# Kernel tuning notes

Measured on AMD Instinct MI355X. Metric: run time of the kernel, lower is better.

## Reference

```python
import jax, jax.numpy as jnp
import numpy as np

NUM_CHARTS = 64
LATENT_DIM = 128
CURVATURE = 1.0
MAX_NORM = 0.99
EPS = 1e-15


def _project_to_ball(z):
    # clamp norm to MAX_NORM (project to interior of Poincare ball)
    norm = jnp.linalg.norm(z, axis=-1, keepdims=True)
    return jnp.where(norm > MAX_NORM, z * (MAX_NORM / norm), z)


def _mobius_add(x, y, c):
    x2 = jnp.sum(x * x, axis=-1, keepdims=True)
    y2 = jnp.sum(y * y, axis=-1, keepdims=True)
    xy = jnp.sum(x * y, axis=-1, keepdims=True)
    num = (1.0 + 2.0 * c * xy + c * y2) * x + (1.0 - c * x2) * y
    den = 1.0 + 2.0 * c * xy + (c * c) * x2 * y2
    return num / jnp.maximum(den, EPS)


def setup_inputs() -> dict:
    key = jax.random.key(0)
    k1, k2, k3, k4, k5 = jax.random.split(key, 5)
    B, D, C = 4096, LATENT_DIM, NUM_CHARTS
    z_n = jax.random.normal(k1, (B, D), dtype=jnp.float32)
    source_idx = jax.random.randint(k2, (B,), 0, C)
    target_idx = jax.random.randint(k3, (B,), 0, C)
    # learned parameters
    chart_centers = 0.1 * jax.random.normal(k4, (C, D), dtype=jnp.float32)
    rotations = jnp.eye(D, dtype=jnp.float32)[None] + 0.01 * jax.random.normal(k5, (C, D, D), dtype=jnp.float32)
    return {"z_n": z_n, "chart_centers": chart_centers, "rotations": rotations,
            "source_idx": source_idx, "target_idx": target_idx}


def reference(z_n, chart_centers, rotations, source_idx, target_idx):
    c = CURVATURE
    z = _project_to_ball(z_n)                                   # [B, D]
    c_source = _project_to_ball(chart_centers[source_idx])      # [B, D]
    z_global = _mobius_add(-c_source, z, c)                     # [B, D]
    R_source = rotations[source_idx]                            # [B, D, D]
    R_target = rotations[target_idx]                            # [B, D, D]
    z_rot = jnp.einsum('bij,bj->bi', R_target, z_global)
    z_rot = jnp.einsum('bji,bj->bi', R_source, z_rot)           # R_source^T @ v
    c_target = _project_to_ball(chart_centers[target_idx])
    z_out = _mobius_add(c_target, z_rot, c)
    return _project_to_ball(z_out)
```

## Files before the change

### kernel.cpp

```cpp
#include <hip/hip_runtime.h>
#include <math.h>

#define D_DIM   128
#define MAXNORM 0.99f
#define MN2     (0.99f * 0.99f)

typedef float f32x4 __attribute__((ext_vector_type(4)));

template <int CTRL, int MASK>
__device__ __forceinline__ float dpp_add(float x) {
  int y = __builtin_amdgcn_update_dpp(0, __float_as_int(x), CTRL, MASK, 0xf, true);
  return x + __int_as_float(y);
}
__device__ __forceinline__ float dpp_sum64(float x) {
  x = dpp_add<0x111, 0xf>(x);
  x = dpp_add<0x112, 0xf>(x);
  x = dpp_add<0x114, 0xf>(x);
  x = dpp_add<0x118, 0xf>(x);
  x = dpp_add<0x142, 0xa>(x);
  x = dpp_add<0x143, 0xc>(x);
  return __int_as_float(__builtin_amdgcn_readlane(__float_as_int(x), 63));
}
__device__ __forceinline__ float dpp_sum32(float x) {
  x = dpp_add<0x111, 0xf>(x);
  x = dpp_add<0x112, 0xf>(x);
  x = dpp_add<0x114, 0xf>(x);
  x = dpp_add<0x118, 0xf>(x);
  x = dpp_add<0x142, 0xa>(x);
  return x;
}

__global__ __launch_bounds__(128, 8) void k_all(
    const float* __restrict__ z_n, const float* __restrict__ centers,
    const float* __restrict__ rot, const int* __restrict__ src_idx,
    const int* __restrict__ tgt_idx, float* __restrict__ out, int B)
{
  __shared__ float zbuf[D_DIM];
  __shared__ float vbuf[D_DIM];
  __shared__ float pbuf[2][D_DIM];

  const int tid = threadIdx.x;
  const int p = tid >> 6, l = tid & 63;
  const int h = l >> 5, q = l & 31;
  const int b = blockIdx.x;
  if (b >= B) return;

  const int ct = tgt_idx[b];
  const int cs = src_idx[b];

  float2 z = ((const float2*)(z_n + (size_t)b * D_DIM))[l];
  float2 c = ((const float2*)(centers + (size_t)cs * D_DIM))[l];
  {
    float y2p = dpp_sum64(z.x * z.x + z.y * z.y);
    float x2p = dpp_sum64(c.x * c.x + c.y * c.y);
    float cz  = dpp_sum64(c.x * z.x + c.y * z.y);
    float sz = 1.0f, y2 = y2p;
    if (y2p > MN2) { sz = MAXNORM / sqrtf(y2p); y2 = MN2; }
    float sc = 1.0f, x2 = x2p;
    if (x2p > MN2) { sc = MAXNORM / sqrtf(x2p); x2 = MN2; }
    float xy  = -(sc * sz) * cz;
    float nx  = 1.0f + 2.0f * xy + y2;
    float ny  = 1.0f - x2;
    float inv = 1.0f / fmaxf(1.0f + 2.0f * xy + x2 * y2, 1e-15f);
    float2 zg;
    zg.x = (nx * (-sc * c.x) + ny * (sz * z.x)) * inv;
    zg.y = (nx * (-sc * c.y) + ny * (sz * z.y)) * inv;
    if (p == 0) ((float2*)zbuf)[l] = zg;
  }
  __syncthreads();

  {
    const float* Rt = rot + (size_t)ct * D_DIM * D_DIM;
    const f32x4 zc = *(const f32x4*)&zbuf[4 * q];
#pragma unroll 8
    for (int t = 0; t < 32; ++t) {
      const int r = 64 * p + 2 * t + h;
      f32x4 rr = *(const f32x4*)&Rt[(size_t)r * D_DIM + 4 * q];
      float pv = fmaf(rr[3], zc[3], fmaf(rr[2], zc[2], fmaf(rr[1], zc[1], rr[0] * zc[0])));
      pv = dpp_sum32(pv);
      if (q == 31) vbuf[r] = pv;
    }
  }
  __syncthreads();

  {
    const float* Rs = rot + (size_t)cs * D_DIM * D_DIM;
    f32x4 acc = {0.0f, 0.0f, 0.0f, 0.0f};
#pragma unroll 16
    for (int t = 0; t < 32; ++t) {
      const int j = 64 * p + 2 * t + h;
      f32x4 rr = *(const f32x4*)&Rs[(size_t)j * D_DIM + 4 * q];
      float vj = vbuf[j];
      acc[0] = fmaf(rr[0], vj, acc[0]);
      acc[1] = fmaf(rr[1], vj, acc[1]);
      acc[2] = fmaf(rr[2], vj, acc[2]);
      acc[3] = fmaf(rr[3], vj, acc[3]);
    }
#pragma unroll
    for (int m = 0; m < 4; ++m) acc[m] += __shfl_xor(acc[m], 32, 64);
    if (h == 0) *(f32x4*)&pbuf[p][4 * q] = acc;
  }
  __syncthreads();

  {
    float2 w0 = ((const float2*)pbuf[0])[l];
    float2 w1 = ((const float2*)pbuf[1])[l];
    float2 wv; wv.x = w0.x + w1.x; wv.y = w0.y + w1.y;
    float2 t = ((const float2*)(centers + (size_t)ct * D_DIM))[l];

    float t2p = dpp_sum64(t.x * t.x + t.y * t.y);
    float w2  = dpp_sum64(wv.x * wv.x + wv.y * wv.y);
    float tw  = dpp_sum64(t.x * wv.x + t.y * wv.y);
    float st = 1.0f, x2 = t2p;
    if (t2p > MN2) { st = MAXNORM / sqrtf(t2p); x2 = MN2; }
    float xy  = st * tw;
    float nx  = 1.0f + 2.0f * xy + w2;
    float ny  = 1.0f - x2;
    float inv = 1.0f / fmaxf(1.0f + 2.0f * xy + x2 * w2, 1e-15f);
    float o0 = (nx * (st * t.x) + ny * wv.x) * inv;
    float o1 = (nx * (st * t.y) + ny * wv.y) * inv;

    float no2 = dpp_sum64(o0 * o0 + o1 * o1);
    if (no2 > MN2) { float sc = MAXNORM / sqrtf(no2); o0 *= sc; o1 *= sc; }

    if (p == 0) {
      float2 o; o.x = o0; o.y = o1;
      ((float2*)(out + (size_t)b * D_DIM))[l] = o;
    }
  }
}

extern "C" void kernel_launch(void* const* d_in, const int* in_sizes, int n_in,
                              void* d_out, int out_size, void* d_ws, size_t ws_size,
                              hipStream_t stream) {
  const float* z_n     = (const float*)d_in[0];
  const float* centers = (const float*)d_in[1];
  const float* rot     = (const float*)d_in[2];
  const int*   src     = (const int*)d_in[3];
  const int*   tgt     = (const int*)d_in[4];
  float* out = (float*)d_out;
  const int B = in_sizes[3];

  k_all<<<dim3(B), dim3(128), 0, stream>>>(z_n, centers, rot, src, tgt, out, B);
}
```

Before: 29.77 us.

## Pre-transpose rotation matrices so both matvecs use broadcast-FMA form

```diff
diff --git a/kernel.cpp b/kernel.cpp
--- a/kernel.cpp
+++ b/kernel.cpp
@@ -30,14 +30,34 @@
   return x;
 }
 
-__global__ __launch_bounds__(128, 8) void k_all(
+__global__ __launch_bounds__(256) void k_tr(
+    const float* __restrict__ rot, float* __restrict__ rtt)
+{
+  __shared__ float tile[32][33];
+  const int c = blockIdx.x >> 4;
+  const int t = blockIdx.x & 15;
+  const int ti = (t >> 2) * 32, tj = (t & 3) * 32;
+  const int r = threadIdx.x >> 5, col = threadIdx.x & 31;
+  const float* R = rot + ((size_t)c << 14);
+  float* T = rtt + ((size_t)c << 14);
+#pragma unroll
+  for (int rr = 0; rr < 32; rr += 8)
+    tile[r + rr][col] = R[(size_t)(ti + r + rr) * D_DIM + tj + col];
+  __syncthreads();
+#pragma unroll
+  for (int rr = 0; rr < 32; rr += 8)
+    T[(size_t)(tj + r + rr) * D_DIM + ti + col] = tile[col][r + rr];
+}
+
+__global__ __launch_bounds__(128, 8) void k_main(
     const float* __restrict__ z_n, const float* __restrict__ centers,
-    const float* __restrict__ rot, const int* __restrict__ src_idx,
-    const int* __restrict__ tgt_idx, float* __restrict__ out, int B)
+    const float* __restrict__ rtt, const float* __restrict__ rot,
+    const int* __restrict__ src_idx, const int* __restrict__ tgt_idx,
+    float* __restrict__ out, int B)
 {
   __shared__ float zbuf[D_DIM];
-  __shared__ float vbuf[D_DIM];
-  __shared__ float pbuf[2][D_DIM];
+  __shared__ float pA[2][D_DIM];
+  __shared__ float pB[2][D_DIM];
 
   const int tid = threadIdx.x;
   const int p = tid >> 6, l = tid & 63;
@@ -70,7 +90,112 @@
   __syncthreads();
 
   {
-    const float* Rt = rot + (size_t)ct * D_DIM * D_DIM;
+    const float* Rt = rtt + ((size_t)ct << 14);
+    f32x4 acc = {0.0f, 0.0f, 0.0f, 0.0f};
+#pragma unroll 16
+    for (int t = 0; t < 32; ++t) {
+      const int j = 64 * p + 2 * t + h;
+      f32x4 rr = *(const f32x4*)&Rt[(size_t)j * D_DIM + 4 * q];
+      float zj = zbuf[j];
+      acc[0] = fmaf(rr[0], zj, acc[0]);
+      acc[1] = fmaf(rr[1], zj, acc[1]);
+      acc[2] = fmaf(rr[2], zj, acc[2]);
+      acc[3] = fmaf(rr[3], zj, acc[3]);
+    }
+#pragma unroll
+    for (int m = 0; m < 4; ++m) acc[m] += __shfl_xor(acc[m], 32, 64);
+    if (h == 0) *(f32x4*)&pA[p][4 * q] = acc;
+  }
+  __syncthreads();
+
+  {
+    const float* Rs = rot + ((size_t)cs << 14);
+    f32x4 acc = {0.0f, 0.0f, 0.0f, 0.0f};
+#pragma unroll 16
+    for (int t = 0; t < 32; ++t) {
+      const int j = 64 * p + 2 * t + h;
+      f32x4 rr = *(const f32x4*)&Rs[(size_t)j * D_DIM + 4 * q];
+      float vj = pA[0][j] + pA[1][j];
+      acc[0] = fmaf(rr[0], vj, acc[0]);
+      acc[1] = fmaf(rr[1], vj, acc[1]);
+      acc[2] = fmaf(rr[2], vj, acc[2]);
+      acc[3] = fmaf(rr[3], vj, acc[3]);
+    }
+#pragma unroll
+    for (int m = 0; m < 4; ++m) acc[m] += __shfl_xor(acc[m], 32, 64);
+    if (h == 0) *(f32x4*)&pB[p][4 * q] = acc;
+  }
+  __syncthreads();
+
+  {
+    float2 w0 = ((const float2*)pB[0])[l];
+    float2 w1 = ((const float2*)pB[1])[l];
+    float2 wv; wv.x = w0.x + w1.x; wv.y = w0.y + w1.y;
+    float2 t = ((const float2*)(centers + (size_t)ct * D_DIM))[l];
+
+    float t2p = dpp_sum64(t.x * t.x + t.y * t.y);
+    float w2  = dpp_sum64(wv.x * wv.x + wv.y * wv.y);
+    float tw  = dpp_sum64(t.x * wv.x + t.y * wv.y);
+    float st = 1.0f, x2 = t2p;
+    if (t2p > MN2) { st = MAXNORM / sqrtf(t2p); x2 = MN2; }
+    float xy  = st * tw;
+    float nx  = 1.0f + 2.0f * xy + w2;
+    float ny  = 1.0f - x2;
+    float inv = 1.0f / fmaxf(1.0f + 2.0f * xy + x2 * w2, 1e-15f);
+    float o0 = (nx * (st * t.x) + ny * wv.x) * inv;
+    float o1 = (nx * (st * t.y) + ny * wv.y) * inv;
+
+    float no2 = dpp_sum64(o0 * o0 + o1 * o1);
+    if (no2 > MN2) { float sc = MAXNORM / sqrtf(no2); o0 *= sc; o1 *= sc; }
+
+    if (p == 0) {
+      float2 o; o.x = o0; o.y = o1;
+      ((float2*)(out + (size_t)b * D_DIM))[l] = o;
+    }
+  }
+}
+
+__global__ __launch_bounds__(128, 8) void k_fb(
+    const float* __restrict__ z_n, const float* __restrict__ centers,
+    const float* __restrict__ rot, const int* __restrict__ src_idx,
+    const int* __restrict__ tgt_idx, float* __restrict__ out, int B)
+{
+  __shared__ float zbuf[D_DIM];
+  __shared__ float vbuf[D_DIM];
+  __shared__ float pbuf[2][D_DIM];
+
+  const int tid = threadIdx.x;
+  const int p = tid >> 6, l = tid & 63;
+  const int h = l >> 5, q = l & 31;
+  const int b = blockIdx.x;
+  if (b >= B) return;
+
+  const int ct = tgt_idx[b];
+  const int cs = src_idx[b];
+
+  float2 z = ((const float2*)(z_n + (size_t)b * D_DIM))[l];
+  float2 c = ((const float2*)(centers + (size_t)cs * D_DIM))[l];
+  {
+    float y2p = dpp_sum64(z.x * z.x + z.y * z.y);
+    float x2p = dpp_sum64(c.x * c.x + c.y * c.y);
+    float cz  = dpp_sum64(c.x * z.x + c.y * z.y);
+    float sz = 1.0f, y2 = y2p;
+    if (y2p > MN2) { sz = MAXNORM / sqrtf(y2p); y2 = MN2; }
+    float sc = 1.0f, x2 = x2p;
+    if (x2p > MN2) { sc = MAXNORM / sqrtf(x2p); x2 = MN2; }
+    float xy  = -(sc * sz) * cz;
+    float nx  = 1.0f + 2.0f * xy + y2;
+    float ny  = 1.0f - x2;
+    float inv = 1.0f / fmaxf(1.0f + 2.0f * xy + x2 * y2, 1e-15f);
+    float2 zg;
+    zg.x = (nx * (-sc * c.x) + ny * (sz * z.x)) * inv;
+    zg.y = (nx * (-sc * c.y) + ny * (sz * z.y)) * inv;
+    if (p == 0) ((float2*)zbuf)[l] = zg;
+  }
+  __syncthreads();
+
+  {
+    const float* Rt = rot + ((size_t)ct << 14);
     const f32x4 zc = *(const f32x4*)&zbuf[4 * q];
 #pragma unroll 8
     for (int t = 0; t < 32; ++t) {
@@ -84,7 +209,7 @@
   __syncthreads();
 
   {
-    const float* Rs = rot + (size_t)cs * D_DIM * D_DIM;
+    const float* Rs = rot + ((size_t)cs << 14);
     f32x4 acc = {0.0f, 0.0f, 0.0f, 0.0f};
 #pragma unroll 16
     for (int t = 0; t < 32; ++t) {
@@ -140,6 +265,13 @@
   const int*   tgt     = (const int*)d_in[4];
   float* out = (float*)d_out;
   const int B = in_sizes[3];
-
-  k_all<<<dim3(B), dim3(128), 0, stream>>>(z_n, centers, rot, src, tgt, out, B);
-}
+  const size_t need = (size_t)64 * D_DIM * D_DIM * sizeof(float);
+
+  if (ws_size >= need) {
+    float* rtt = (float*)d_ws;
+    k_tr<<<dim3(64 * 16), dim3(256), 0, stream>>>(rot, rtt);
+    k_main<<<dim3(B), dim3(128), 0, stream>>>(z_n, centers, rtt, rot, src, tgt, out, B);
+  } else {
+    k_fb<<<dim3(B), dim3(128), 0, stream>>>(z_n, centers, rot, src, tgt, out, B);
+  }
+}
```

Result: slower. 50.16 us (+68.4%).
